# Performance work log

Hardware: AMD Instinct MI355X
Metric: run time of the kernel (lower is better)

The kernel has to match this reference:

```python
import jax, jax.numpy as jnp
import numpy as np

N_HEAD = 8
HEAD_DIM = 64
DIM = 512
INNER = N_HEAD * HEAD_DIM
ATT_THRESHOLD = 1e-4
SCALE = HEAD_DIM ** -0.5


def setup_inputs() -> dict:
    key = jax.random.key(0)
    ks = jax.random.split(key, 7)
    b, n, dn = 2, 2048, 2048
    fr = jax.random.normal(ks[0], (b, n, DIM), dtype=jnp.float32)
    dt = jax.random.normal(ks[1], (b, dn, DIM), dtype=jnp.float32)
    s = DIM ** -0.5
    Wq = jax.random.normal(ks[2], (DIM, INNER), dtype=jnp.float32) * s
    Wk = jax.random.normal(ks[3], (DIM, INNER), dtype=jnp.float32) * s
    Wv = jax.random.normal(ks[4], (DIM, INNER), dtype=jnp.float32) * s
    Wo = jax.random.normal(ks[5], (INNER, DIM), dtype=jnp.float32) * (INNER ** -0.5)
    bo = jax.random.normal(ks[6], (DIM,), dtype=jnp.float32) * 0.01
    return {"fr": fr, "dt": dt, "Wq": Wq, "Wk": Wk, "Wv": Wv, "Wo": Wo, "bo": bo}


def reference(fr, dt, Wq, Wk, Wv, Wo, bo):
    b, n, _ = fr.shape
    dn = dt.shape[1]
    # projections -> [b, seq, n_head, head_dim]
    q = (fr @ Wq).reshape(b, n, N_HEAD, HEAD_DIM)
    k = (dt @ Wk).reshape(b, dn, N_HEAD, HEAD_DIM)
    v = (dt @ Wv).reshape(b, dn, N_HEAD, HEAD_DIM)
    # full attention matrix [b, h, n, dn]
    scores = jnp.einsum('bihd,bjhd->bhij', q, k) * SCALE
    attn = jax.nn.softmax(scores, axis=-1)
    # torch .clip(t) with one positional arg clamps the MIN: max(attn, t)
    attn = jnp.maximum(attn, ATT_THRESHOLD) - ATT_THRESHOLD
    attn = attn / jnp.sum(attn, axis=-1, keepdims=True)
    out = jnp.einsum('bhij,bjhd->bihd', attn, v).reshape(b, n, INNER)
    return out @ Wo + bo
```

## Files before the change

kernel.cpp:

```cpp
#include <hip/hip_runtime.h>
#include <hip/hip_bf16.h>

#define BB 2
#define SEQ 2048
#define NHEAD 8
#define HD 64
#define ATT_T 1e-4f
#define QSCALE 0.18033688011112042f

typedef short s16x8 __attribute__((ext_vector_type(8)));
typedef float f32x16 __attribute__((ext_vector_type(16)));

#define MFMA32(a, b, c) __builtin_amdgcn_mfma_f32_32x32x16_bf16((a), (b), (c), 0, 0, 0)
#define EXP2(x) __builtin_amdgcn_exp2f(x)
#define SB0() __builtin_amdgcn_sched_barrier(0)
#define WAITVM0() __builtin_amdgcn_s_waitcnt(0x0F70)
#define WAITVM4() __builtin_amdgcn_s_waitcnt(0x0F74)
#define WAITVM8() __builtin_amdgcn_s_waitcnt(0x0F78)
#define WAITVM12() __builtin_amdgcn_s_waitcnt(0x0F7C)

__device__ __forceinline__ unsigned short bfr(float x) {
  __hip_bfloat16 h = __float2bfloat16(x);
  return __builtin_bit_cast(unsigned short, h);
}
__device__ __forceinline__ unsigned int packbf(float a, float b) {
  return (unsigned int)bfr(a) | ((unsigned int)bfr(b) << 16);
}
__device__ __forceinline__ unsigned int permpack(float a, float b) {
  return __builtin_amdgcn_perm(__builtin_bit_cast(unsigned int, b),
                               __builtin_bit_cast(unsigned int, a), 0x07060302u);
}
__device__ __forceinline__ void async16(const void* g, void* l) {
  __builtin_amdgcn_global_load_lds(
      (const __attribute__((address_space(1))) unsigned int*)g,
      (__attribute__((address_space(3))) unsigned int*)l, 16, 0, 0);
}
__device__ __forceinline__ void plswap(unsigned a, unsigned b, int lh,
                                       unsigned& x, unsigned& z) {
#if __has_builtin(__builtin_amdgcn_permlane32_swap)
  typedef unsigned uint2v __attribute__((ext_vector_type(2)));
  uint2v r = __builtin_amdgcn_permlane32_swap(a, b, false, false);
  x = r[0];
  z = r[1];
#else
  unsigned ea = (unsigned)__shfl_xor((int)a, 32);
  unsigned eb = (unsigned)__shfl_xor((int)b, 32);
  x = lh ? eb : a;
  z = lh ? b : ea;
#endif
}


__global__ __launch_bounds__(256) void prep(const float* __restrict__ fr,
                                            const float* __restrict__ dt,
                                            const float* __restrict__ w0,
                                            const float* __restrict__ w1,
                                            const float* __restrict__ w2,
                                            const float* __restrict__ w3,
                                            unsigned short* __restrict__ frB,
                                            unsigned short* __restrict__ dtB,
                                            unsigned short* __restrict__ o0,
                                            unsigned short* __restrict__ o1,
                                            unsigned short* __restrict__ o2,
                                            unsigned short* __restrict__ o3) {
  const int bid = blockIdx.x;
  if (bid < 2048) {
    const float* src = (bid < 1024) ? fr : dt;
    unsigned short* dst = (bid < 1024) ? frB : dtB;
    const int chunk = (bid < 1024) ? bid : bid - 1024;
    const size_t base = (size_t)chunk * 2048 + threadIdx.x * 8;
    float4 a = *(const float4*)(src + base);
    float4 b = *(const float4*)(src + base + 4);
    uint4 o;
    o.x = packbf(a.x, a.y);
    o.y = packbf(a.z, a.w);
    o.z = packbf(b.x, b.y);
    o.w = packbf(b.z, b.w);
    *(uint4*)(dst + base) = o;
    return;
  }
  __shared__ float tle[64][65];
  const int t = bid - 2048;
  const int z = t >> 6, by = (t >> 3) & 7, bx = t & 7;
  const float* W = z == 0 ? w0 : z == 1 ? w1 : z == 2 ? w2 : w3;
  unsigned short* WT = z == 0 ? o0 : z == 1 ? o1 : z == 2 ? o2 : o3;
  const int r0 = by * 64, c0 = bx * 64;
  const int tr = threadIdx.x >> 4;
  const int tc = threadIdx.x & 15;
  #pragma unroll
  for (int i = 0; i < 4; i++) {
    int r = tr + i * 16;
    float4 v = *(const float4*)(W + (size_t)(r0 + r) * 512 + c0 + tc * 4);
    tle[r][tc * 4 + 0] = v.x;
    tle[r][tc * 4 + 1] = v.y;
    tle[r][tc * 4 + 2] = v.z;
    tle[r][tc * 4 + 3] = v.w;
  }
  __syncthreads();
  #pragma unroll
  for (int i = 0; i < 4; i++) {
    int c = tr + i * 16;
    int rr = tc * 4;
    uint2 p;
    p.x = packbf(tle[rr + 0][c], tle[rr + 1][c]);
    p.y = packbf(tle[rr + 2][c], tle[rr + 3][c]);
    *(uint2*)(WT + (size_t)(c0 + c) * 512 + r0 + rr) = p;
  }
}

__global__ __launch_bounds__(256) void gemm_qkv(const unsigned short* __restrict__ frB,
                                                const unsigned short* __restrict__ dtB,
                                                const unsigned short* __restrict__ WqT,
                                                const unsigned short* __restrict__ WkT,
                                                const unsigned short* __restrict__ WvT,
                                                unsigned short* __restrict__ Qp,
                                                unsigned short* __restrict__ Kp,
                                                unsigned short* __restrict__ VTp) {
  __shared__ __align__(16) unsigned short smem[24576];
  unsigned short* Asm = smem;
  unsigned short* Bsm = smem + 8192;
  const int tid = threadIdx.x, lane = tid & 63, w = tid >> 6;
  const int l31 = lane & 31, lh = lane >> 5;
  const int m0 = blockIdx.y * 64, n0 = blockIdx.x * 128;
  const int z = blockIdx.z;
  const unsigned short* Ab = z == 0 ? frB : dtB;
  const unsigned short* BT = z == 0 ? WqT : (z == 1 ? WkT : WvT);
  unsigned short* OP = z == 0 ? Qp : (z == 1 ? Kp : VTp);
  const float scale = z == 0 ? QSCALE : 1.0f;

  const int rl = lane >> 3;
  const int cl8 = ((lane & 7) ^ rl) * 8;
  const int x7 = l31 & 7;

  auto stage = [&](int kt, int buf) {
    const int k0 = kt * 64;
    #pragma unroll
    for (int i = 0; i < 2; i++) {
      int s = w * 2 + i;
      async16(Ab + (size_t)(m0 + s * 8 + rl) * 512 + k0 + cl8,
              Asm + buf * 4096 + s * 512);
    }
    #pragma unroll
    for (int i = 0; i < 4; i++) {
      int s = w * 4 + i;
      async16(BT + (size_t)(n0 + s * 8 + rl) * 512 + k0 + cl8,
              Bsm + buf * 8192 + s * 512);
    }
  };

  f32x16 acc[2];
  #pragma unroll
  for (int j = 0; j < 2; j++)
    #pragma unroll
    for (int r = 0; r < 16; r++) acc[j][r] = 0.f;

  stage(0, 0);
  for (int kt = 0; kt < 8; ++kt) {
    __syncthreads();
    if (kt + 1 < 8) stage(kt + 1, (kt + 1) & 1);
    const int buf = kt & 1;
    const unsigned short* as = Asm + buf * 4096 + ((w & 1) * 32 + l31) * 64;
    const unsigned short* bs = Bsm + buf * 8192 + ((w >> 1) * 64 + l31) * 64;
    #pragma unroll
    for (int ks = 0; ks < 4; ++ks) {
      const int co = ((ks * 2 + lh) ^ x7) * 8;
      s16x8 af = *(const s16x8*)(as + co);
      s16x8 b0 = *(const s16x8*)(bs + co);
      s16x8 b1 = *(const s16x8*)(bs + 2048 + co);
      acc[0] = MFMA32(af, b0, acc[0]);
      acc[1] = MFMA32(af, b1, acc[1]);
    }
  }

  const int wm = (w & 1) * 32, wn = (w >> 1) * 64;
  const int bb = m0 >> 11, s0 = m0 & 2047;
  __syncthreads();
  if (z <= 1) {
    #pragma unroll
    for (int j = 0; j < 2; j++)
      #pragma unroll
      for (int r = 0; r < 16; r++) {
        int mm = wm + (r & 3) + 8 * (r >> 2) + 4 * lh;
        int nn = wn + j * 32 + l31;
        smem[mm * 136 + nn] = bfr(acc[j][r] * scale);
      }
    __syncthreads();
    #pragma unroll
    for (int it = 0; it < 4; ++it) {
      int c = tid + it * 256;
      int mm = c >> 4, seg = c & 15;
      uint4 vdat = *(const uint4*)(smem + mm * 136 + seg * 8);
      int n = n0 + seg * 8, h = n >> 6, d = n & 63;
      *(uint4*)(OP + ((size_t)((bb * NHEAD + h) * SEQ + s0 + mm)) * HD + d) = vdat;
    }
  } else {
    #pragma unroll
    for (int j = 0; j < 2; j++)
      #pragma unroll
      for (int r = 0; r < 16; r += 2) {
        int mm = wm + (r & 3) + 8 * (r >> 2) + 4 * lh;
        int nn = wn + j * 32 + l31;
        *(unsigned int*)(smem + nn * 72 + mm) = packbf(acc[j][r], acc[j][r + 1]);
      }
    __syncthreads();
    #pragma unroll
    for (int it = 0; it < 4; ++it) {
      int c = tid + it * 256;
      int nn = c >> 3, seg = c & 7;
      uint4 vdat = *(const uint4*)(smem + nn * 72 + seg * 8);
      int n = n0 + nn, h = n >> 6, d = n & 63;
      *(uint4*)(OP + ((size_t)((bb * NHEAD + h) * HD + d)) * SEQ + s0 + seg * 8) = vdat;
    }
  }
}

__global__ __launch_bounds__(256) void gemm_out(const unsigned short* __restrict__ A,
                                                const unsigned short* __restrict__ BT,
                                                const float* __restrict__ bias,
                                                float* __restrict__ O) {
  __shared__ __align__(16) unsigned short smem[16384];
  unsigned short* Asm = smem;
  unsigned short* Bsm = smem + 8192;
  const int tid = threadIdx.x, lane = tid & 63, w = tid >> 6;
  const int l31 = lane & 31, lh = lane >> 5;
  const int m0 = blockIdx.y * 64, n0 = blockIdx.x * 64;

  const int rl = lane >> 3;
  const int cl8 = ((lane & 7) ^ rl) * 8;
  const int x7 = l31 & 7;

  auto stage = [&](int kt, int buf) {
    const int k0 = kt * 64;
    #pragma unroll
    for (int i = 0; i < 2; i++) {
      int s = w * 2 + i;
      async16(A + (size_t)(m0 + s * 8 + rl) * 512 + k0 + cl8,
              Asm + buf * 4096 + s * 512);
      async16(BT + (size_t)(n0 + s * 8 + rl) * 512 + k0 + cl8,
              Bsm + buf * 4096 + s * 512);
    }
  };

  f32x16 acc;
  #pragma unroll
  for (int r = 0; r < 16; r++) acc[r] = 0.f;

  stage(0, 0);
  for (int kt = 0; kt < 8; ++kt) {
    __syncthreads();
    if (kt + 1 < 8) stage(kt + 1, (kt + 1) & 1);
    const int buf = kt & 1;
    const unsigned short* as = Asm + buf * 4096 + ((w & 1) * 32 + l31) * 64;
    const unsigned short* bs = Bsm + buf * 4096 + ((w >> 1) * 32 + l31) * 64;
    #pragma unroll
    for (int ks = 0; ks < 4; ++ks) {
      const int co = ((ks * 2 + lh) ^ x7) * 8;
      s16x8 af = *(const s16x8*)(as + co);
      s16x8 bf = *(const s16x8*)(bs + co);
      acc = MFMA32(af, bf, acc);
    }
  }

  const int wm = (w & 1) * 32, wn = (w >> 1) * 32;
  float bv = bias[n0 + wn + l31];
  #pragma unroll
  for (int r = 0; r < 16; r++) {
    int mm = wm + (r & 3) + 8 * (r >> 2) + 4 * lh;
    O[(size_t)(m0 + mm) * 512 + n0 + wn + l31] = acc[r] + bv;
  }
}

__global__ __launch_bounds__(256, 2) void attn_mfma(const unsigned short* __restrict__ Q,
                                                    const unsigned short* __restrict__ K,
                                                    const unsigned short* __restrict__ VT,
                                                    unsigned short* __restrict__ O) {
  __shared__ __align__(16) unsigned short arena[4][8192];
  __shared__ float larr[4][64];
  __shared__ float warr[4][64];

  const int tid = threadIdx.x;
  const int lane = tid & 63;
  const int w = tid >> 6;
  const int l31 = lane & 31, lh = lane >> 5;

  const int bid = blockIdx.x;
  const int g = bid & 7, j = bid >> 3;
  const int bh = g * 2 + (j >> 5);
  const int qt = j & 31;

  const unsigned short* Qh = Q + (size_t)bh * SEQ * HD;
  const unsigned short* Kh = K + (size_t)bh * SEQ * HD;
  const unsigned short* VTh = VT + (size_t)bh * HD * SEQ;

  s16x8 qf[2][4];
  #pragma unroll
  for (int q2 = 0; q2 < 2; q2++)
    #pragma unroll
    for (int t = 0; t < 4; t++)
      qf[q2][t] = *(const s16x8*)(Qh + (size_t)(qt * 64 + q2 * 32 + l31) * HD + 16 * t + 8 * lh);

  unsigned short* kbuf = &arena[w][0];
  const int kbase = w * 512;

  const int rl = lane >> 3;
  const int cl8 = ((lane & 7) ^ rl) * 8;
  const int x7 = l31 & 7;

  auto stageK = [&](int c, int slot) {
    const unsigned short* G = Kh + (size_t)(kbase + c * 32 + rl) * HD + cl8;
    #pragma unroll
    for (int tt = 0; tt < 4; tt++)
      async16(G + tt * 512, kbuf + slot * 2048 + tt * 512);
  };

  f32x16 scp[2];
  auto qkt = [&](int slot) {
    const unsigned short* kb = kbuf + slot * 2048 + l31 * 64;
    s16x8 kf[4];
    #pragma unroll
    for (int tt = 0; tt < 4; tt++)
      kf[tt] = *(const s16x8*)(kb + ((tt * 2 + lh) ^ x7) * 8);
    #pragma unroll
    for (int q2 = 0; q2 < 2; q2++) {
      f32x16 sc;
      #pragma unroll
      for (int r = 0; r < 16; r++) sc[r] = 0.f;
      #pragma unroll
      for (int tt = 0; tt < 4; tt++) sc = MFMA32(kf[tt], qf[q2][tt], sc);
      scp[q2] = sc;
    }
  };

  float lsum[2] = {0.f, 0.f};
  auto accum_l = [&]() {
    #pragma unroll
    for (int q2 = 0; q2 < 2; q2++) {
      float s0 = 0.f, s1 = 0.f, s2 = 0.f, s3 = 0.f;
      #pragma unroll
      for (int r = 0; r < 4; r++) {
        s0 += EXP2(scp[q2][r]);
        s1 += EXP2(scp[q2][4 + r]);
        s2 += EXP2(scp[q2][8 + r]);
        s3 += EXP2(scp[q2][12 + r]);
      }
      lsum[q2] += (s0 + s1) + (s2 + s3);
    }
  };

  stageK(0, 0);
  stageK(1, 1);
  stageK(2, 2);
  for (int c = 0; c < 16; ++c) {
    if (c + 3 < 16) stageK(c + 3, (c + 3) & 3);
    if (c > 0) accum_l();
    if (c < 13) { WAITVM12(); }
    else if (c == 13) { WAITVM8(); }
    else if (c == 14) { WAITVM4(); }
    else { WAITVM0(); }
    SB0();
    qkt(c & 3);
  }
  accum_l();
  #pragma unroll
  for (int q2 = 0; q2 < 2; q2++) lsum[q2] += __shfl_xor(lsum[q2], 32);
  if (lh == 0) { larr[w][l31] = lsum[0]; larr[w][32 + l31] = lsum[1]; }
  __syncthreads();
  float tl[2];
  #pragma unroll
  for (int q2 = 0; q2 < 2; q2++)
    tl[q2] = ATT_T * (larr[0][q2 * 32 + l31] + larr[1][q2 * 32 + l31] +
                      larr[2][q2 * 32 + l31] + larr[3][q2 * 32 + l31]);

  f32x16 acc[2][2];
  #pragma unroll
  for (int q2 = 0; q2 < 2; q2++)
    #pragma unroll
    for (int dh = 0; dh < 2; dh++)
      #pragma unroll
      for (int r = 0; r < 16; r++) acc[q2][dh][r] = 0.f;
  float wacc[2] = {0.f, 0.f};
  s16x8 vrA[4], vrB[4];

  auto loadV = [&](int c, s16x8(&vr)[4]) {
    #pragma unroll
    for (int dh = 0; dh < 2; dh++)
      #pragma unroll
      for (int kc = 0; kc < 2; kc++)
        vr[dh * 2 + kc] = *(const s16x8*)(VTh + (size_t)(dh * 32 + l31) * SEQ +
                                          kbase + c * 32 + kc * 16 + lh * 8);
  };
  auto softmax_pv = [&](const s16x8(&vr)[4]) {
    s16x8 pf[2][2];
    #pragma unroll
    for (int q2 = 0; q2 < 2; q2++) {
      uint2 quads[4];
      #pragma unroll
      for (int gq = 0; gq < 4; gq++) {
        float u0 = fmaxf(EXP2(scp[q2][4 * gq + 0]) - tl[q2], 0.f);
        float u1 = fmaxf(EXP2(scp[q2][4 * gq + 1]) - tl[q2], 0.f);
        float u2 = fmaxf(EXP2(scp[q2][4 * gq + 2]) - tl[q2], 0.f);
        float u3 = fmaxf(EXP2(scp[q2][4 * gq + 3]) - tl[q2], 0.f);
        wacc[q2] += (u0 + u1) + (u2 + u3);
        quads[gq].x = permpack(u0, u1);
        quads[gq].y = permpack(u2, u3);
      }
      #pragma unroll
      for (int tp = 0; tp < 2; tp++) {
        unsigned x0, z0, x1, z1;
        plswap(quads[2 * tp].x, quads[2 * tp + 1].x, lh, x0, z0);
        plswap(quads[2 * tp].y, quads[2 * tp + 1].y, lh, x1, z1);
        uint4 fr;
        fr.x = x0; fr.y = x1; fr.z = z0; fr.w = z1;
        pf[q2][tp] = __builtin_bit_cast(s16x8, fr);
      }
    }
    #pragma unroll
    for (int q2 = 0; q2 < 2; q2++)
      #pragma unroll
      for (int dh = 0; dh < 2; dh++) {
        acc[q2][dh] = MFMA32(pf[q2][0], vr[dh * 2 + 0], acc[q2][dh]);
        acc[q2][dh] = MFMA32(pf[q2][1], vr[dh * 2 + 1], acc[q2][dh]);
      }
  };

  stageK(0, 0);
  stageK(1, 1);
  stageK(2, 2);
  loadV(0, vrA);
  for (int cc = 0; cc < 16; cc += 2) {
    if (cc > 0) {
      if (cc < 14) { WAITVM12(); } else { WAITVM8(); }
      SB0();
      softmax_pv(vrB);
    }
    loadV(cc + 1, vrB);
    if (cc + 3 < 16) stageK(cc + 3, (cc + 3) & 3);
    if (cc == 0) { WAITVM12(); }
    SB0();
    qkt(cc & 3);
    if (cc == 0) { WAITVM8(); }
    else if (cc < 14) { WAITVM12(); }
    else { WAITVM4(); }
    SB0();
    softmax_pv(vrA);
    if (cc + 2 < 16) loadV(cc + 2, vrA);
    if (cc + 4 < 16) stageK(cc + 4, (cc + 4) & 3);
    SB0();
    qkt((cc + 1) & 3);
  }
  WAITVM0();
  SB0();
  softmax_pv(vrB);

  #pragma unroll
  for (int q2 = 0; q2 < 2; q2++) wacc[q2] += __shfl_xor(wacc[q2], 32);
  if (lh == 0) { warr[w][l31] = wacc[0]; warr[w][32 + l31] = wacc[1]; }
  __syncthreads();

  float* plane0 = (float*)&arena[0][0];
  float* plane1 = (float*)&arena[1][0];

  if (w >= 2) {
    float* pl = (w == 2) ? plane0 : plane1;
    #pragma unroll
    for (int q2 = 0; q2 < 2; q2++)
      #pragma unroll
      for (int dh = 0; dh < 2; dh++)
        #pragma unroll
        for (int r = 0; r < 16; r++) {
          int ql = q2 * 32 + (r & 3) + 8 * (r >> 2) + 4 * lh;
          pl[ql * 64 + dh * 32 + l31] = acc[q2][dh][r];
        }
  }
  __syncthreads();
  if (w < 2) {
    float* pl = (w == 0) ? plane0 : plane1;
    #pragma unroll
    for (int q2 = 0; q2 < 2; q2++)
      #pragma unroll
      for (int dh = 0; dh < 2; dh++)
        #pragma unroll
        for (int r = 0; r < 16; r++) {
          int ql = q2 * 32 + (r & 3) + 8 * (r >> 2) + 4 * lh;
          acc[q2][dh][r] += pl[ql * 64 + dh * 32 + l31];
        }
  }
  __syncthreads();
  if (w == 1) {
    #pragma unroll
    for (int q2 = 0; q2 < 2; q2++)
      #pragma unroll
      for (int dh = 0; dh < 2; dh++)
        #pragma unroll
        for (int r = 0; r < 16; r++) {
          int ql = q2 * 32 + (r & 3) + 8 * (r >> 2) + 4 * lh;
          plane0[ql * 64 + dh * 32 + l31] = acc[q2][dh][r];
        }
  }
  __syncthreads();
  unsigned short* otile = &arena[2][0];
  if (w == 0) {
    #pragma unroll
    for (int q2 = 0; q2 < 2; q2++)
      #pragma unroll
      for (int dh = 0; dh < 2; dh++)
        #pragma unroll
        for (int r = 0; r < 16; r++) {
          int ql = q2 * 32 + (r & 3) + 8 * (r >> 2) + 4 * lh;
          float wt = warr[0][ql] + warr[1][ql] + warr[2][ql] + warr[3][ql];
          float v = (acc[q2][dh][r] + plane0[ql * 64 + dh * 32 + l31]) / wt;
          otile[ql * 64 + dh * 32 + l31] = bfr(v);
        }
  }
  __syncthreads();
  const int b = bh >> 3, h = bh & 7;
  #pragma unroll
  for (int it = 0; it < 2; ++it) {
    int c2 = tid + it * 256;
    int mm = c2 >> 3, seg = c2 & 7;
    uint4 vdat = *(const uint4*)(otile + mm * 64 + seg * 8);
    *(uint4*)(O + ((size_t)(b * SEQ + qt * 64 + mm)) * 512 + h * HD + seg * 8) = vdat;
  }
}

extern "C" void kernel_launch(void* const* d_in, const int* in_sizes, int n_in,
                              void* d_out, int out_size, void* d_ws, size_t ws_size,
                              hipStream_t stream) {
  const float* fr = (const float*)d_in[0];
  const float* dt = (const float*)d_in[1];
  const float* Wq = (const float*)d_in[2];
  const float* Wk = (const float*)d_in[3];
  const float* Wv = (const float*)d_in[4];
  const float* Wo = (const float*)d_in[5];
  const float* bo = (const float*)d_in[6];
  float* out = (float*)d_out;

  const size_t planeE = (size_t)BB * SEQ * 512;
  const size_t wE = 512 * 512;
  unsigned short* p = (unsigned short*)d_ws;
  unsigned short* WqT = p; p += wE;
  unsigned short* WkT = p; p += wE;
  unsigned short* WvT = p; p += wE;
  unsigned short* WoT = p; p += wE;
  unsigned short* Qp  = p; p += planeE;
  unsigned short* Kp  = p; p += planeE;
  unsigned short* VTp = p; p += planeE;
  unsigned short* aoB = p; p += planeE;

  unsigned short* frB = (unsigned short*)d_out;
  unsigned short* dtB = (unsigned short*)d_out + planeE;

  prep<<<2304, 256, 0, stream>>>(fr, dt, Wq, Wk, Wv, Wo, frB, dtB, WqT, WkT, WvT, WoT);

  gemm_qkv<<<dim3(4, 64, 3), 256, 0, stream>>>(frB, dtB, WqT, WkT, WvT, Qp, Kp, VTp);

  attn_mfma<<<BB * NHEAD * 32, 256, 0, stream>>>(Qp, Kp, VTp, aoB);

  gemm_out<<<dim3(8, 64), 256, 0, stream>>>(aoB, WoT, bo, out);
}
```

Baseline: 143.2 us.

## Store Q/K/V in MFMA fragment-packed layout for contiguous attention loads

The projection GEMM epilogue now writes Q, K and V^T tiles in a pre-swizzled, fragment-ordered layout, where each 32-row chunk of a head is stored as a contiguous 2048-element block ordered by lane. The attention kernel can then load Q fragments, stage K, and load V with fully contiguous lane*8 addressing. This drops the XOR swizzle and strided row gathers, which is meant to improve global coalescing and LDS access. The cost is a more complex scatter in the GEMM epilogue and a tight coupling between the producer and consumer layouts.

Result: faster. 137.9 us (median of 2 runs) (-3.7%).

```diff
diff --git a/kernel.cpp b/kernel.cpp
--- a/kernel.cpp
+++ b/kernel.cpp
@@ -174,6 +174,7 @@
 
   const int wm = (w & 1) * 32, wn = (w >> 1) * 64;
   const int bb = m0 >> 11, s0 = m0 & 2047;
+  const int h0 = n0 >> 6, cbase = s0 >> 5;
   __syncthreads();
   if (z <= 1) {
     #pragma unroll
@@ -187,11 +188,14 @@
     __syncthreads();
     #pragma unroll
     for (int it = 0; it < 4; ++it) {
-      int c = tid + it * 256;
-      int mm = c >> 4, seg = c & 15;
-      uint4 vdat = *(const uint4*)(smem + mm * 136 + seg * 8);
-      int n = n0 + seg * 8, h = n >> 6, d = n & 63;
-      *(uint4*)(OP + ((size_t)((bb * NHEAD + h) * SEQ + s0 + mm)) * HD + d) = vdat;
+      int u = tid + it * 256;
+      int b = u >> 8, v = u & 255;
+      int hp = b >> 1, cp = b & 1;
+      int mm = cp * 32 + (v & 31);
+      int nn = hp * 64 + ((v >> 6) << 4) + (((v >> 5) & 1) << 3);
+      uint4 vdat = *(const uint4*)(smem + mm * 136 + nn);
+      *(uint4*)(OP + ((size_t)(bb * NHEAD + h0 + hp)) * SEQ * HD +
+                (size_t)(cbase + cp) * 2048 + v * 8) = vdat;
     }
   } else {
     #pragma unroll
@@ -205,11 +209,15 @@
     __syncthreads();
     #pragma unroll
     for (int it = 0; it < 4; ++it) {
-      int c = tid + it * 256;
-      int nn = c >> 3, seg = c & 7;
-      uint4 vdat = *(const uint4*)(smem + nn * 72 + seg * 8);
-      int n = n0 + nn, h = n >> 6, d = n & 63;
-      *(uint4*)(OP + ((size_t)((bb * NHEAD + h) * HD + d)) * SEQ + s0 + seg * 8) = vdat;
+      int u = tid + it * 256;
+      int hp = u >> 9;
+      int rem = u & 511;
+      int cp = rem >> 8, v = rem & 255;
+      int nn = hp * 64 + ((v >> 7) << 5) + (v & 31);
+      int mm0 = cp * 32 + (((v >> 6) & 1) << 4) + (((v >> 5) & 1) << 3);
+      uint4 vdat = *(const uint4*)(smem + nn * 72 + mm0);
+      *(uint4*)(OP + ((size_t)(bb * NHEAD + h0 + hp)) * SEQ * HD +
+                (size_t)(cbase + cp) * 2048 + v * 8) = vdat;
     }
   }
 }
@@ -290,24 +298,19 @@
 
   const unsigned short* Qh = Q + (size_t)bh * SEQ * HD;
   const unsigned short* Kh = K + (size_t)bh * SEQ * HD;
-  const unsigned short* VTh = VT + (size_t)bh * HD * SEQ;
+  const unsigned short* VTh = VT + (size_t)bh * SEQ * HD;
 
   s16x8 qf[2][4];
   #pragma unroll
   for (int q2 = 0; q2 < 2; q2++)
     #pragma unroll
     for (int t = 0; t < 4; t++)
-      qf[q2][t] = *(const s16x8*)(Qh + (size_t)(qt * 64 + q2 * 32 + l31) * HD + 16 * t + 8 * lh);
+      qf[q2][t] = *(const s16x8*)(Qh + (size_t)(qt * 2 + q2) * 2048 + t * 512 + lane * 8);
 
   unsigned short* kbuf = &arena[w][0];
-  const int kbase = w * 512;
-
-  const int rl = lane >> 3;
-  const int cl8 = ((lane & 7) ^ rl) * 8;
-  const int x7 = l31 & 7;
 
   auto stageK = [&](int c, int slot) {
-    const unsigned short* G = Kh + (size_t)(kbase + c * 32 + rl) * HD + cl8;
+    const unsigned short* G = Kh + (size_t)(w * 16 + c) * 2048 + lane * 8;
     #pragma unroll
     for (int tt = 0; tt < 4; tt++)
       async16(G + tt * 512, kbuf + slot * 2048 + tt * 512);
@@ -315,11 +318,10 @@
 
   f32x16 scp[2];
   auto qkt = [&](int slot) {
-    const unsigned short* kb = kbuf + slot * 2048 + l31 * 64;
     s16x8 kf[4];
     #pragma unroll
     for (int tt = 0; tt < 4; tt++)
-      kf[tt] = *(const s16x8*)(kb + ((tt * 2 + lh) ^ x7) * 8);
+      kf[tt] = *(const s16x8*)(kbuf + slot * 2048 + tt * 512 + lane * 8);
     #pragma unroll
     for (int q2 = 0; q2 < 2; q2++) {
       f32x16 sc;
@@ -382,12 +384,10 @@
   s16x8 vrA[4], vrB[4];
 
   auto loadV = [&](int c, s16x8(&vr)[4]) {
-    #pragma unroll
-    for (int dh = 0; dh < 2; dh++)
-      #pragma unroll
-      for (int kc = 0; kc < 2; kc++)
-        vr[dh * 2 + kc] = *(const s16x8*)(VTh + (size_t)(dh * 32 + l31) * SEQ +
-                                          kbase + c * 32 + kc * 16 + lh * 8);
+    const unsigned short* G = VTh + (size_t)(w * 16 + c) * 2048 + lane * 8;
+    #pragma unroll
+    for (int jj = 0; jj < 4; jj++)
+      vr[jj] = *(const s16x8*)(G + jj * 512);
   };
   auto softmax_pv = [&](const s16x8(&vr)[4]) {
     s16x8 pf[2][2];
```
